# Performance work log

Measured on AMD Instinct MI355X. Metric: run time of the kernel, lower is better.

The kernel has to match this reference:

```python
import jax, jax.numpy as jnp
import numpy as np

HEADS = 16

def setup_inputs() -> dict:
    key = jax.random.key(0)
    k1, k2, k3 = jax.random.split(key, 3)
    b, t, d = 2, 2048, 1024
    x = jax.random.normal(k1, (b, t, d), dtype=jnp.float32)
    w_qkv = jax.random.normal(k2, (d, 3 * d), dtype=jnp.float32) * (d ** -0.5)
    w_out = jax.random.normal(k3, (d, d), dtype=jnp.float32) * (d ** -0.5)
    b_out = jnp.zeros((d,), dtype=jnp.float32)
    return {"x": x, "w_qkv": w_qkv, "w_out": w_out, "b_out": b_out}

def reference(x, w_qkv, w_out, b_out):
    b, t, d = x.shape
    h = HEADS
    dh = d // h
    qkv = x @ w_qkv                      # [b, t, 3d]
    q, k, v = jnp.split(qkv, 3, axis=-1)
    split_heads = lambda a: a.reshape(b, t, h, dh).transpose(0, 2, 1, 3)  # [b,h,t,dh]
    q, k, v = map(split_heads, (q, k, v))
    # NOTE: faithful to source — no 1/sqrt(dh) scaling, causal=False so no mask
    dots = jnp.einsum('bhid,bhjd->bhij', q, k)      # [b,h,t,t]
    attn = jax.nn.softmax(dots, axis=-1)
    out = jnp.einsum('bhjd,bhij->bhid', v, attn)    # [b,h,t,dh]
    out = out.transpose(0, 2, 1, 3).reshape(b, t, d)
    return out @ w_out + b_out
```

## Files before the change

kernel.cpp:

```cpp
#include <hip/hip_runtime.h>
#include <hip/hip_bf16.h>
#include <stdint.h>

typedef __attribute__((ext_vector_type(4))) float f32x4;
typedef __attribute__((ext_vector_type(8))) short bf16x8;

#define MFMA(a, b, c) __builtin_amdgcn_mfma_f32_16x16x32_bf16((a), (b), (c), 0, 0, 0)
#define BAR do { __builtin_amdgcn_s_barrier(); asm volatile("" ::: "memory"); } while (0)

template <int N> __device__ __forceinline__ void waitcnt_vm() {
  if constexpr (N == 0) asm volatile("s_waitcnt vmcnt(0)" ::: "memory");
  else if constexpr (N == 3) asm volatile("s_waitcnt vmcnt(3)" ::: "memory");
  else if constexpr (N == 4) asm volatile("s_waitcnt vmcnt(4)" ::: "memory");
}

__device__ __forceinline__ uint16_t f2b(float f) {
  uint32_t u = __builtin_bit_cast(uint32_t, f);
  uint32_t r = (u + 0x7FFFu + ((u >> 16) & 1u)) >> 16;
  return (uint16_t)r;
}

__device__ __forceinline__ uint32_t cvt_pk_bf16(float lo, float hi) {
  uint32_t r;
  asm("v_cvt_pk_bf16_f32 %0, %1, %2" : "=v"(r) : "v"(lo), "v"(hi));
  return r;
}

__device__ __forceinline__ float fexp2(float x) {
  float r;
  asm("v_exp_f32 %0, %1" : "=v"(r) : "v"(x));
  return r;
}

__device__ __forceinline__ void gld_lds16(const void* g, void* l) {
  __builtin_amdgcn_global_load_lds((const __attribute__((address_space(1))) uint32_t*)g,
                                   (__attribute__((address_space(3))) uint32_t*)l, 16, 0, 0);
}

__device__ __forceinline__ int swz(int r) {
  return (r & 3) | ((((r >> 2) ^ (r >> 3)) & 1) << 2);
}

__global__ __launch_bounds__(256) void cast_bf16(const float* __restrict__ in,
                                                 uint16_t* __restrict__ out, int n) {
  const int i = (blockIdx.x * 256 + threadIdx.x) * 4;
  if (i >= n) return;
  const float4 v = *(const float4*)(in + i);
  ushort4 o;
  o.x = f2b(v.x); o.y = f2b(v.y); o.z = f2b(v.z); o.w = f2b(v.w);
  *(ushort4*)(out + i) = o;
}

__global__ __launch_bounds__(256) void transpose_cast(const float* __restrict__ in,
                                                      uint16_t* __restrict__ out, int R, int C) {
  __shared__ float t_[32][33];
  const int c0 = blockIdx.x * 32, r0 = blockIdx.y * 32;
  const int tx = threadIdx.x & 31, ty = threadIdx.x >> 5;
#pragma unroll
  for (int i = 0; i < 4; i++)
    t_[ty + i * 8][tx] = in[(size_t)(r0 + ty + i * 8) * C + c0 + tx];
  __syncthreads();
#pragma unroll
  for (int i = 0; i < 4; i++)
    out[(size_t)(c0 + ty + i * 8) * R + r0 + tx] = f2b(t_[tx][ty + i * 8]);
}

template <int NOUT, int BN, bool BF16_OUT, bool BIAS, bool SCALEQ, bool VSPLIT>
__global__ __launch_bounds__(256) void gemm_bt(const uint16_t* __restrict__ A,
                                               const uint16_t* __restrict__ Bt,
                                               const float* __restrict__ bias,
                                               void* __restrict__ Cout,
                                               uint16_t* __restrict__ VTout) {
  constexpr int NF = BN / 32;
  constexpr int TILEB = 8192 + BN * 64;
  constexpr int NL = 2 + BN / 64;
  __shared__ __align__(16) char LDS[3 * TILEB];
  const int tid = threadIdx.x;
  const int wave = tid >> 6, lane = tid & 63;
  const int lr = lane & 15, lg = lane >> 4;
  const int row0 = blockIdx.y * 128, col0 = blockIdx.x * BN;
  const int wr = (wave >> 1) * 64, wc = (wave & 1) * (BN / 2);

  f32x4 acc[4][NF] = {};

  const int ldsOff = wave * 1024 + lane * 16;
  const int srow = ldsOff >> 6, scolB = ldsOff & 63;
  const char* ApA = (const char*)A + ((size_t)(row0 + srow) * 1024) * 2 + scolB;
  const char* ApB = ApA + 64 * 2048;
  const char* BpA = (const char*)Bt + ((size_t)(col0 + srow) * 1024) * 2 + scolB;
  const char* BpB = BpA + 64 * 2048;

  auto stage = [&](int t, char* base) {
    char* d = base + wave * 1024;
    const int kk = t * 64;
    gld_lds16(ApA + kk, d);
    gld_lds16(ApB + kk, d + 4096);
    gld_lds16(BpA + kk, d + 8192);
    if constexpr (BN == 128) gld_lds16(BpB + kk, d + 12288);
  };
  auto compute = [&](const char* S) {
    bf16x8 af[4], bfv[NF];
#pragma unroll
    for (int i = 0; i < 4; i++)
      af[i] = *(const bf16x8*)(S + (wr + i * 16 + lr) * 64 + lg * 16);
#pragma unroll
    for (int j = 0; j < NF; j++)
      bfv[j] = *(const bf16x8*)(S + 8192 + (wc + j * 16 + lr) * 64 + lg * 16);
    __builtin_amdgcn_s_setprio(1);
#pragma unroll
    for (int i = 0; i < 4; i++)
#pragma unroll
      for (int j = 0; j < NF; j++)
        acc[i][j] = MFMA(af[i], bfv[j], acc[i][j]);
    __builtin_amdgcn_s_setprio(0);
  };

  stage(0, LDS);
  stage(1, LDS + TILEB);
#pragma unroll 1
  for (int i = 0; i < 30; i += 3) {
    waitcnt_vm<NL>(); BAR; stage(i + 2, LDS + 2 * TILEB); compute(LDS);
    waitcnt_vm<NL>(); BAR; stage(i + 3, LDS);             compute(LDS + TILEB);
    waitcnt_vm<NL>(); BAR; stage(i + 4, LDS + TILEB);     compute(LDS + 2 * TILEB);
  }
  waitcnt_vm<NL>(); BAR; compute(LDS);
  waitcnt_vm<0>();  BAR; compute(LDS + TILEB);

  const float qs = (SCALEQ && col0 < 1024) ? 1.4426950408889634f : 1.0f;
#pragma unroll
  for (int i = 0; i < 4; i++)
#pragma unroll
    for (int j = 0; j < NF; j++) {
      const int col = col0 + wc + j * 16 + lr;
      const int rowb = row0 + wr + i * 16 + lg * 4;
      if (VSPLIT && col >= 2048) {
        ushort4 vs;
        vs.x = f2b(acc[i][j][0]); vs.y = f2b(acc[i][j][1]);
        vs.z = f2b(acc[i][j][2]); vs.w = f2b(acc[i][j][3]);
        const int bIdx = rowb >> 11, tok = rowb & 2047;
        *(ushort4*)(VTout + (size_t)(bIdx * 1024 + (col - 2048)) * 2048 + tok) = vs;
      } else {
        const float bv = BIAS ? bias[col] : 0.f;
#pragma unroll
        for (int r = 0; r < 4; r++) {
          const float v = acc[i][j][r] * qs + bv;
          if (BF16_OUT) ((uint16_t*)Cout)[(size_t)(rowb + r) * NOUT + col] = f2b(v);
          else          ((float*)Cout)[(size_t)(rowb + r) * NOUT + col] = v;
        }
      }
    }
}

__global__ __launch_bounds__(256) void attn_fwd(const uint16_t* __restrict__ qkv,
                                                const uint16_t* __restrict__ VT,
                                                uint16_t* __restrict__ O) {
  __shared__ __align__(16) char LDS[2 * 16384];
  const int tid = threadIdx.x;
  const int wave = tid >> 6, lane = tid & 63;
  const int lr = lane & 15, lg = lane >> 4;
  const int id = blockIdx.x;
  const int w = id >> 3;
  const int bh = (id & 7) * 4 + (w >> 5);
  const int qt = w & 31;
  const int b = bh >> 4, h = bh & 15;
  const int q0 = qt * 64 + wave * 16;

  const uint16_t* Qp = qkv + (size_t)(b * 2048 + q0 + lr) * 3072 + h * 64 + lg * 8;
  const bf16x8 qf0 = *(const bf16x8*)Qp;
  const bf16x8 qf1 = *(const bf16x8*)(Qp + 32);

  const int off1 = wave * 1024 + lane * 16;
  const int off2 = off1 + 4096;
  const int r1 = off1 >> 7, c1 = (off1 >> 4) & 7;
  const int r2 = off2 >> 7, c2 = (off2 >> 4) & 7;
  const char* qb = (const char*)qkv;
  const char* vb = (const char*)VT;
  const char* Kp1 = qb + ((size_t)(b * 2048 + r1) * 3072 + 1024 + h * 64) * 2 + (c1 ^ swz(r1)) * 16;
  const char* Kp2 = qb + ((size_t)(b * 2048 + r2) * 3072 + 1024 + h * 64) * 2 + (c2 ^ swz(r2)) * 16;
  const char* Vp1 = vb + ((size_t)(bh * 64 + r1) * 2048) * 2 + (c1 ^ swz(r1)) * 16;
  const char* Vp2 = vb + ((size_t)(bh * 64 + r2) * 2048) * 2 + (c2 ^ swz(r2)) * 16;

  const int wb1 = wave * 1024;
  const int wb2 = 4096 + wave * 1024;

  auto stage = [&](size_t t, char* slot) {
    const size_t ka = t * 393216;
    const int va = (int)t * 128;
    gld_lds16(Kp1 + ka, slot + wb1);
    gld_lds16(Kp2 + ka, slot + wb2);
    gld_lds16(Vp1 + va, slot + 8192 + wb1);
    gld_lds16(Vp2 + va, slot + 8192 + wb2);
  };

  int koff[8], voff[8];
  const int rbase = ((lr >> 2) << 3) | (lr & 3);
#pragma unroll
  for (int fj = 0; fj < 4; fj++) {
    const int row = rbase + ((fj & 1) << 2) + ((fj >> 1) << 5);
    const int sw = swz(row);
    koff[fj * 2]     = row * 128 + ((lg ^ sw) * 16);
    koff[fj * 2 + 1] = row * 128 + (((4 + lg) ^ sw) * 16);
  }
#pragma unroll
  for (int cf = 0; cf < 4; cf++) {
    const int dr = cf * 16 + lr;
    const int sw = swz(dr);
    voff[cf * 2]     = 8192 + dr * 128 + ((lg ^ sw) * 16);
    voff[cf * 2 + 1] = 8192 + dr * 128 + (((4 + lg) ^ sw) * 16);
  }

  f32x4 o[4] = {};
  float l_ = 0.f;
  const char* ldsB = (const char*)LDS;

  auto compute = [&](int sb) {
    f32x4 s[4] = {};
    __builtin_amdgcn_s_setprio(1);
#pragma unroll
    for (int fj = 0; fj < 4; fj++) {
      const bf16x8 k0 = *(const bf16x8*)(ldsB + sb + koff[fj * 2]);
      const bf16x8 k1 = *(const bf16x8*)(ldsB + sb + koff[fj * 2 + 1]);
      s[fj] = MFMA(k0, qf0, s[fj]);
      s[fj] = MFMA(k1, qf1, s[fj]);
    }
    __builtin_amdgcn_s_setprio(0);
    union PW { uint32_t u[8]; struct { bf16x8 a0, a1; } f; } pw;
#pragma unroll
    for (int fj = 0; fj < 4; fj++) {
      const float p0 = fexp2(s[fj][0]), p1 = fexp2(s[fj][1]);
      const float p2 = fexp2(s[fj][2]), p3 = fexp2(s[fj][3]);
      l_ += (p0 + p1) + (p2 + p3);
      pw.u[fj * 2]     = cvt_pk_bf16(p0, p1);
      pw.u[fj * 2 + 1] = cvt_pk_bf16(p2, p3);
    }
    __builtin_amdgcn_s_setprio(1);
#pragma unroll
    for (int cf = 0; cf < 4; cf++) {
      const bf16x8 v0 = *(const bf16x8*)(ldsB + sb + voff[cf * 2]);
      const bf16x8 v1 = *(const bf16x8*)(ldsB + sb + voff[cf * 2 + 1]);
      o[cf] = MFMA(pw.f.a0, v0, o[cf]);
      o[cf] = MFMA(pw.f.a1, v1, o[cf]);
    }
    __builtin_amdgcn_s_setprio(0);
  };

  stage(0, LDS);
#pragma unroll 1
  for (int t = 0; t < 30; t += 2) {
    BAR;
    stage(t + 1, LDS + 16384);
    waitcnt_vm<4>(); BAR;
    compute(0);
    BAR;
    stage(t + 2, LDS);
    waitcnt_vm<4>(); BAR;
    compute(16384);
  }
  BAR; stage(31, LDS + 16384);
  waitcnt_vm<4>(); BAR; compute(0);
  waitcnt_vm<0>(); BAR; compute(16384);

  l_ += __shfl_xor(l_, 16, 64);
  l_ += __shfl_xor(l_, 32, 64);

#pragma unroll
  for (int cf = 0; cf < 4; cf++)
#pragma unroll
    for (int r = 0; r < 4; r++) {
      const float lrow = __shfl(l_, lg * 4 + r, 64);
      const float v = o[cf][r] / lrow;
      const int row = b * 2048 + q0 + lg * 4 + r;
      const int col = h * 64 + cf * 16 + lr;
      O[(size_t)row * 1024 + col] = f2b(v);
    }
}

extern "C" void kernel_launch(void* const* d_in, const int* in_sizes, int n_in,
                              void* d_out, int out_size, void* d_ws, size_t ws_size,
                              hipStream_t stream) {
  const float* x    = (const float*)d_in[0];
  const float* wqkv = (const float*)d_in[1];
  const float* wout = (const float*)d_in[2];
  const float* bout = (const float*)d_in[3];

  char* ws = (char*)d_ws;
  uint16_t* woutT   = (uint16_t*)(ws + 0);
  uint16_t* qkvb    = (uint16_t*)(ws + (2ull  << 20));
  uint16_t* VT      = (uint16_t*)(ws + (26ull << 20));
  uint16_t* xb      = (uint16_t*)(ws + (34ull << 20));
  uint16_t* wqkvT   = (uint16_t*)(ws + (42ull << 20));
  uint16_t* attnout = xb;

  cast_bf16<<<dim3(4096), dim3(256), 0, stream>>>(x, xb, 4096 * 1024);
  transpose_cast<<<dim3(96, 32), dim3(256), 0, stream>>>(wqkv, wqkvT, 1024, 3072);
  transpose_cast<<<dim3(32, 32), dim3(256), 0, stream>>>(wout, woutT, 1024, 1024);

  gemm_bt<3072, 128, true, false, true, true>
      <<<dim3(24, 32), dim3(256), 0, stream>>>(xb, wqkvT, nullptr, qkvb, VT);
  attn_fwd<<<dim3(1024), dim3(256), 0, stream>>>(qkvb, VT, attnout);
  gemm_bt<1024, 64, false, true, false, false>
      <<<dim3(16, 32), dim3(256), 0, stream>>>(attnout, woutT, bout, d_out, nullptr);
}
```

Before: 121.1 us.

## Process two 16-row query tiles per wave in attention to reuse K/V loads

Each wave now handles 32 query rows (two 16-row MFMA tiles) instead of 16, so each attention block covers 128 queries and the grid is halved to 512 blocks. K and V fragments read from LDS and staged from global memory are reused across both query tiles, halving K/V traffic per unit of work. The cost is doubled accumulator and score registers per wave and fewer blocks to fill the 256 CUs, which may reduce occupancy and load balance.

```diff
diff --git a/kernel.cpp b/kernel.cpp
--- a/kernel.cpp
+++ b/kernel.cpp
@@ -160,14 +160,16 @@
   const int lr = lane & 15, lg = lane >> 4;
   const int id = blockIdx.x;
   const int w = id >> 3;
-  const int bh = (id & 7) * 4 + (w >> 5);
-  const int qt = w & 31;
+  const int bh = (id & 7) * 4 + (w >> 4);
+  const int qt = w & 15;
   const int b = bh >> 4, h = bh & 15;
-  const int q0 = qt * 64 + wave * 16;
+  const int q0 = qt * 128 + wave * 32;
 
   const uint16_t* Qp = qkv + (size_t)(b * 2048 + q0 + lr) * 3072 + h * 64 + lg * 8;
-  const bf16x8 qf0 = *(const bf16x8*)Qp;
-  const bf16x8 qf1 = *(const bf16x8*)(Qp + 32);
+  const bf16x8 qA0 = *(const bf16x8*)Qp;
+  const bf16x8 qA1 = *(const bf16x8*)(Qp + 32);
+  const bf16x8 qB0 = *(const bf16x8*)(Qp + 16 * 3072);
+  const bf16x8 qB1 = *(const bf16x8*)(Qp + 16 * 3072 + 32);
 
   const int off1 = wave * 1024 + lane * 16;
   const int off2 = off1 + 4096;
@@ -209,37 +211,48 @@
     voff[cf * 2 + 1] = 8192 + dr * 128 + (((4 + lg) ^ sw) * 16);
   }
 
-  f32x4 o[4] = {};
-  float l_ = 0.f;
+  f32x4 oA[4] = {}, oB[4] = {};
+  float lA = 0.f, lB = 0.f;
   const char* ldsB = (const char*)LDS;
 
+  union PW { uint32_t u[8]; struct { bf16x8 a0, a1; } f; };
+
   auto compute = [&](int sb) {
-    f32x4 s[4] = {};
+    f32x4 s0[4] = {}, s1[4] = {};
     __builtin_amdgcn_s_setprio(1);
 #pragma unroll
     for (int fj = 0; fj < 4; fj++) {
       const bf16x8 k0 = *(const bf16x8*)(ldsB + sb + koff[fj * 2]);
       const bf16x8 k1 = *(const bf16x8*)(ldsB + sb + koff[fj * 2 + 1]);
-      s[fj] = MFMA(k0, qf0, s[fj]);
-      s[fj] = MFMA(k1, qf1, s[fj]);
+      s0[fj] = MFMA(k0, qA0, s0[fj]);
+      s0[fj] = MFMA(k1, qA1, s0[fj]);
+      s1[fj] = MFMA(k0, qB0, s1[fj]);
+      s1[fj] = MFMA(k1, qB1, s1[fj]);
     }
     __builtin_amdgcn_s_setprio(0);
-    union PW { uint32_t u[8]; struct { bf16x8 a0, a1; } f; } pw;
+    PW pA, pB;
 #pragma unroll
     for (int fj = 0; fj < 4; fj++) {
-      const float p0 = fexp2(s[fj][0]), p1 = fexp2(s[fj][1]);
-      const float p2 = fexp2(s[fj][2]), p3 = fexp2(s[fj][3]);
-      l_ += (p0 + p1) + (p2 + p3);
-      pw.u[fj * 2]     = cvt_pk_bf16(p0, p1);
-      pw.u[fj * 2 + 1] = cvt_pk_bf16(p2, p3);
+      const float a0 = fexp2(s0[fj][0]), a1 = fexp2(s0[fj][1]);
+      const float a2 = fexp2(s0[fj][2]), a3 = fexp2(s0[fj][3]);
+      lA += (a0 + a1) + (a2 + a3);
+      pA.u[fj * 2]     = cvt_pk_bf16(a0, a1);
+      pA.u[fj * 2 + 1] = cvt_pk_bf16(a2, a3);
+      const float b0 = fexp2(s1[fj][0]), b1 = fexp2(s1[fj][1]);
+      const float b2 = fexp2(s1[fj][2]), b3 = fexp2(s1[fj][3]);
+      lB += (b0 + b1) + (b2 + b3);
+      pB.u[fj * 2]     = cvt_pk_bf16(b0, b1);
+      pB.u[fj * 2 + 1] = cvt_pk_bf16(b2, b3);
     }
     __builtin_amdgcn_s_setprio(1);
 #pragma unroll
     for (int cf = 0; cf < 4; cf++) {
       const bf16x8 v0 = *(const bf16x8*)(ldsB + sb + voff[cf * 2]);
       const bf16x8 v1 = *(const bf16x8*)(ldsB + sb + voff[cf * 2 + 1]);
-      o[cf] = MFMA(pw.f.a0, v0, o[cf]);
-      o[cf] = MFMA(pw.f.a1, v1, o[cf]);
+      oA[cf] = MFMA(pA.f.a0, v0, oA[cf]);
+      oA[cf] = MFMA(pA.f.a1, v1, oA[cf]);
+      oB[cf] = MFMA(pB.f.a0, v0, oB[cf]);
+      oB[cf] = MFMA(pB.f.a1, v1, oB[cf]);
     }
     __builtin_amdgcn_s_setprio(0);
   };
@@ -260,18 +273,19 @@
   waitcnt_vm<4>(); BAR; compute(0);
   waitcnt_vm<0>(); BAR; compute(16384);
 
-  l_ += __shfl_xor(l_, 16, 64);
-  l_ += __shfl_xor(l_, 32, 64);
+  lA += __shfl_xor(lA, 16, 64); lA += __shfl_xor(lA, 32, 64);
+  lB += __shfl_xor(lB, 16, 64); lB += __shfl_xor(lB, 32, 64);
 
 #pragma unroll
   for (int cf = 0; cf < 4; cf++)
 #pragma unroll
     for (int r = 0; r < 4; r++) {
-      const float lrow = __shfl(l_, lg * 4 + r, 64);
-      const float v = o[cf][r] / lrow;
-      const int row = b * 2048 + q0 + lg * 4 + r;
+      const float la = __shfl(lA, lg * 4 + r, 64);
+      const float lb = __shfl(lB, lg * 4 + r, 64);
       const int col = h * 64 + cf * 16 + lr;
-      O[(size_t)row * 1024 + col] = f2b(v);
+      const int rowA = b * 2048 + q0 + lg * 4 + r;
+      O[(size_t)rowA * 1024 + col] = f2b(oA[cf][r] / la);
+      O[(size_t)(rowA + 16) * 1024 + col] = f2b(oB[cf][r] / lb);
     }
 }
 
@@ -297,7 +311,7 @@
 
   gemm_bt<3072, 128, true, false, true, true>
       <<<dim3(24, 32), dim3(256), 0, stream>>>(xb, wqkvT, nullptr, qkvb, VT);
-  attn_fwd<<<dim3(1024), dim3(256), 0, stream>>>(qkvb, VT, attnout);
+  attn_fwd<<<dim3(512), dim3(256), 0, stream>>>(qkvb, VT, attnout);
   gemm_bt<1024, 64, false, true, false, false>
       <<<dim3(16, 32), dim3(256), 0, stream>>>(attnout, woutT, bout, d_out, nullptr);
 }
```

Result: faster. 113.8 us (-6.0%).
